# Optimization experiments

Measured on AMD Instinct MI355X. Metric: run time of the kernel, lower is better.

Reference implementation:

```python
import jax, jax.numpy as jnp
import numpy as np
from jax import lax

M = 8   # num_heads
K = 4   # num_points


def conv2d(x, w, b, pad):
    # x: [B,C,H,W], w: [O,I,kh,kw]
    y = lax.conv_general_dilated(x, w, (1, 1), [(pad, pad), (pad, pad)],
                                 dimension_numbers=('NCHW', 'OIHW', 'NCHW'))
    return y + b[None, :, None, None]


def grid_sample_zeros(v, px, py):
    # Bilinear grid_sample, align_corners=True, padding_mode='zeros'.
    # v: [N,Cm,H,W]; px,py: [N,P] in pixel coordinates.
    N, Cm, H, W = v.shape
    x0 = jnp.floor(px); y0 = jnp.floor(py)
    x1 = x0 + 1.0;      y1 = y0 + 1.0
    wx = px - x0;       wy = py - y0
    vflat = v.reshape(N, Cm, H * W)

    def tap(xi, yi):
        valid = (xi >= 0) & (xi <= W - 1) & (yi >= 0) & (yi <= H - 1)
        xc = jnp.clip(xi, 0, W - 1).astype(jnp.int32)
        yc = jnp.clip(yi, 0, H - 1).astype(jnp.int32)
        idx = yc * W + xc                          # [N,P]
        g = jnp.take_along_axis(vflat, idx[:, None, :], axis=2)  # [N,Cm,P]
        return g * valid[:, None, :].astype(v.dtype)

    v00 = tap(x0, y0); v01 = tap(x1, y0)
    v10 = tap(x0, y1); v11 = tap(x1, y1)
    wx = wx[:, None, :]; wy = wy[:, None, :]
    return (v00 * (1 - wx) * (1 - wy) + v01 * wx * (1 - wy)
            + v10 * (1 - wx) * wy + v11 * wx * wy)


def setup_inputs() -> dict:
    key = jax.random.key(0)
    ks = jax.random.split(key, 16)
    B, C, H, W = 8, 256, 64, 64
    s = 0.02
    inp = {
        'f_recalib': jax.random.normal(ks[0], (B, C, H, W), jnp.float32),
        'f_orig':    jax.random.normal(ks[1], (B, C, H, W), jnp.float32),
        'offset_w': jax.random.normal(ks[2], (M * K * 2, C, 3, 3), jnp.float32) * s,
        'offset_b': jnp.zeros((M * K * 2,), jnp.float32),
        'attn_w':   jax.random.normal(ks[3], (M * K, C, 3, 3), jnp.float32) * s,
        'attn_b':   jnp.zeros((M * K,), jnp.float32),
        'value_w':  jax.random.normal(ks[4], (C, C, 1, 1), jnp.float32) * s,
        'value_b':  jnp.zeros((C,), jnp.float32),
        'proj_w':   jax.random.normal(ks[5], (C, C, 1, 1), jnp.float32) * s,
        'proj_b':   jnp.zeros((C,), jnp.float32),
        'mlp_w1':   jax.random.normal(ks[6], (2 * C, C, 1, 1), jnp.float32) * s,
        'mlp_b1':   jnp.zeros((2 * C,), jnp.float32),
        'mlp_w2':   jax.random.normal(ks[7], (C, 2 * C, 1, 1), jnp.float32) * s,
        'mlp_b2':   jnp.zeros((C,), jnp.float32),
    }
    return inp


def reference(f_recalib, f_orig, offset_w, offset_b, attn_w, attn_b,
              value_w, value_b, proj_w, proj_b,
              mlp_w1, mlp_b1, mlp_w2, mlp_b2):
    B, C, H, W = f_recalib.shape
    Cm = C // M

    offsets = conv2d(f_recalib, offset_w, offset_b, 1).reshape(B, M, K, 2, H, W)
    attn = conv2d(f_recalib, attn_w, attn_b, 1).reshape(B, M, K, H, W)
    attn = jax.nn.softmax(attn, axis=2)
    value = conv2d(f_recalib, value_w, value_b, 0)

    gy, gx = jnp.meshgrid(jnp.arange(H, dtype=jnp.float32),
                          jnp.arange(W, dtype=jnp.float32), indexing='ij')
    gx_sym = (W - 1) - gx  # horizontally mirrored x coordinate
    # pixel-space sampling locations (align_corners=True normalization is exactly
    # inverted by grid_sample's unnormalization, so work in pixel coords)
    px = gx_sym[None, None, None] + offsets[:, :, :, 0]  # [B,M,K,H,W]
    py = gy[None, None, None] + offsets[:, :, :, 1]

    v = value.reshape(B * M, Cm, H, W)
    sampled = grid_sample_zeros(v, px.reshape(B * M, -1), py.reshape(B * M, -1))
    sampled = sampled.reshape(B, M, Cm, K, H, W)

    out = (sampled * attn[:, :, None]).sum(axis=3).reshape(B, C, H, W)
    out = conv2d(out, proj_w, proj_b, 0) + f_orig
    h = jax.nn.relu(conv2d(out, mlp_w1, mlp_b1, 0))
    out = conv2d(h, mlp_w2, mlp_b2, 0) + out
    return out
```

## Files before the change

### kernel.cpp

```cpp
#include <hip/hip_runtime.h>
#include <cstddef>

#define P_ 4096
#define PW_ 66

using u16 = unsigned short;
typedef float  f32x4  __attribute__((ext_vector_type(4)));
typedef u16    u16x8  __attribute__((ext_vector_type(8)));
typedef u16    u16x4  __attribute__((ext_vector_type(4)));
typedef __bf16 bf16x8 __attribute__((ext_vector_type(8)));

#define DEVINL __device__ __forceinline__

DEVINL u16 f2bf(float f) {
    union { float f; unsigned u; } v; v.f = f;
    unsigned r = v.u + 0x7fffu + ((v.u >> 16) & 1u);
    return (u16)(r >> 16);
}
DEVINL float bf2f(u16 h) {
    union { unsigned u; float f; } v; v.u = ((unsigned)h) << 16;
    return v.f;
}

DEVINL f32x4 mfma16(u16x8 a, u16x8 b, f32x4 c) {
    return __builtin_amdgcn_mfma_f32_16x16x32_bf16(
        __builtin_bit_cast(bf16x8, a), __builtin_bit_cast(bf16x8, b), c, 0, 0, 0);
}

DEVINL void gload16(const u16* src, const u16* lds_dst) {
    __builtin_amdgcn_global_load_lds(
        (const __attribute__((address_space(1))) void*)src,
        (__attribute__((address_space(3))) void*)lds_dst, 16, 0, 0);
}

__global__ void prep_weights(const float* __restrict__ off_w, const float* __restrict__ attn_w,
                             const float* __restrict__ val_w, const float* __restrict__ proj_w,
                             const float* __restrict__ w1, const float* __restrict__ w2,
                             u16* __restrict__ wbf) {
    int idx = blockIdx.x * 256 + threadIdx.x;
    if (idx >= 614400) return;
    float v;
    if (idx < 221184) {
        int tap = idx / 24576, rem = idx - tap * 24576, oc = rem >> 8, ic = rem & 255;
        v = (oc < 64) ? off_w[(size_t)(oc * 256 + ic) * 9 + tap]
                      : attn_w[(size_t)((oc - 64) * 256 + ic) * 9 + tap];
    } else if (idx < 286720) v = val_w[idx - 221184];
    else if (idx < 352256)   v = proj_w[idx - 286720];
    else if (idx < 483328)   v = w1[idx - 352256];
    else                     v = w2[idx - 483328];
    wbf[idx] = f2bf(v);
}

__global__ __launch_bounds__(256) void zero_pad(u16* __restrict__ xp) {
    const int b = blockIdx.x, t = threadIdx.x;
    const u16x8 z = (u16x8){0, 0, 0, 0, 0, 0, 0, 0};
    for (int q = t; q < 8320; q += 256) {
        const int p = q >> 5, chunk = q & 31;
        int row, col;
        if (p < 66)       { row = 0;  col = p; }
        else if (p < 132) { row = 65; col = p - 66; }
        else { const int q2 = p - 132; row = 1 + (q2 >> 1); col = (q2 & 1) * 65; }
        *(u16x8*)&xp[((size_t)(b * PW_ + row) * PW_ + col) * 256 + chunk * 8] = z;
    }
}

__global__ __launch_bounds__(256) void to_nhwc_pad(const float* __restrict__ in,
                                                   u16* __restrict__ xp) {
    const int y = blockIdx.x, c0 = blockIdx.y * 64, b = blockIdx.z;
    __shared__ u16 ts[64 * 72];
    const int t = threadIdx.x, cl = t >> 4, xq = t & 15;
    #pragma unroll
    for (int r = 0; r < 4; ++r) {
        const int c = r * 16 + cl;
        const float4 v = *(const float4*)&in[((size_t)(b * 256 + c0 + c)) * P_ + y * 64 + xq * 4];
        ts[(xq * 4 + 0) * 72 + c] = f2bf(v.x);
        ts[(xq * 4 + 1) * 72 + c] = f2bf(v.y);
        ts[(xq * 4 + 2) * 72 + c] = f2bf(v.z);
        ts[(xq * 4 + 3) * 72 + c] = f2bf(v.w);
    }
    __syncthreads();
    const int px = t >> 2, seg = t & 3;
    u16x8 o0, o1;
    #pragma unroll
    for (int j = 0; j < 8; ++j) {
        o0[j] = ts[px * 72 + seg * 16 + j];
        o1[j] = ts[px * 72 + seg * 16 + 8 + j];
    }
    const size_t base = ((size_t)(b * PW_ + y + 1) * PW_ + 1 + px) * 256 + c0 + seg * 16;
    *(u16x8*)&xp[base]     = o0;
    *(u16x8*)&xp[base + 8] = o1;
}

__global__ __launch_bounds__(256, 4) void conv3x3_mfma(
    const u16* __restrict__ xp, const u16* __restrict__ wconv,
    const float* __restrict__ off_b, const float* __restrict__ attn_b,
    u16* __restrict__ convout) {
    const int y = blockIdx.x, b = blockIdx.y;
    const int tid = threadIdx.x, w = tid >> 6, lane = tid & 63, g = lane >> 4, i = lane & 15;
    const int wm = w & 1, wn = w >> 1;
    const int srow = lane >> 4, sc = lane & 15;
    __shared__ u16 xs[64 * 128];
    __shared__ u16 wsL[96 * 128];

    f32x4 acc[2][3];
    #pragma unroll
    for (int mi = 0; mi < 2; ++mi)
        #pragma unroll
        for (int nj = 0; nj < 3; ++nj) acc[mi][nj] = (f32x4){0.f, 0.f, 0.f, 0.f};

    for (int tap = 0; tap < 9; ++tap) {
        const int dy = tap / 3, dx = tap % 3;
        const u16* xrow = xp + ((size_t)(b * PW_ + y + dy) * PW_ + dx) * 256;
        const u16* wt = wconv + (size_t)(tap * 96) * 256;
        for (int cc = 0; cc < 2; ++cc) {
            const int kc = cc * 128;
            #pragma unroll
            for (int t = 0; t < 4; ++t) {
                const int j = w * 4 + t;
                const int row = j * 4 + srow;
                const int cs = sc ^ (row & 7);
                gload16(xrow + (size_t)row * 256 + kc + (cs << 3), &xs[j * 512]);
            }
            #pragma unroll
            for (int t = 0; t < 6; ++t) {
                const int j = w * 6 + t;
                const int row = j * 4 + srow;
                const int cs = sc ^ (row & 7);
                gload16(wt + (size_t)row * 256 + kc + (cs << 3), &wsL[j * 512]);
            }
            __syncthreads();
            #pragma unroll
            for (int ks = 0; ks < 4; ++ks) {
                u16x8 a[2], bb[3];
                #pragma unroll
                for (int mi = 0; mi < 2; ++mi) {
                    const int pr = wm * 32 + mi * 16 + i;
                    a[mi] = *(const u16x8*)&xs[pr * 128 + (((ks * 4 + g) ^ (pr & 7)) << 3)];
                }
                #pragma unroll
                for (int nj = 0; nj < 3; ++nj) {
                    const int ocr = wn * 48 + nj * 16 + i;
                    bb[nj] = *(const u16x8*)&wsL[ocr * 128 + (((ks * 4 + g) ^ (ocr & 7)) << 3)];
                }
                #pragma unroll
                for (int mi = 0; mi < 2; ++mi)
                    #pragma unroll
                    for (int nj = 0; nj < 3; ++nj)
                        acc[mi][nj] = mfma16(a[mi], bb[nj], acc[mi][nj]);
            }
            __syncthreads();
        }
    }
    #pragma unroll
    for (int mi = 0; mi < 2; ++mi) {
        const int x0 = wm * 32 + mi * 16 + g * 4;
        #pragma unroll
        for (int nj = 0; nj < 3; ++nj) {
            const int oc = wn * 48 + nj * 16 + i;
            const float bv = (oc < 64) ? off_b[oc] : attn_b[oc - 64];
            #pragma unroll
            for (int r = 0; r < 4; ++r)
                convout[((size_t)(b * P_ + y * 64 + x0 + r)) * 96 + oc] =
                    f2bf(acc[mi][nj][r] + bv);
        }
    }
}

__global__ __launch_bounds__(256, 2) void gemm128(
    const u16* __restrict__ X, const u16* __restrict__ W,
    const float* __restrict__ bias, const float* __restrict__ resid,
    void* __restrict__ outp, u16* __restrict__ out_nhwc,
    const int KTOT, const int OC, const int mode, const int padded) {
    const int px0 = blockIdx.x * 128, oc0 = blockIdx.y * 128, b = blockIdx.z;
    const int tid = threadIdx.x, w = tid >> 6, lane = tid & 63, g = lane >> 4, i = lane & 15;
    const int wm = w & 1, wn = w >> 1;
    __shared__ u16 lds[32768];
    u16* xs = lds;
    u16* wsL = lds + 16384;

    f32x4 acc[4][4];
    #pragma unroll
    for (int mi = 0; mi < 4; ++mi)
        #pragma unroll
        for (int nj = 0; nj < 4; ++nj) acc[mi][nj] = (f32x4){0.f, 0.f, 0.f, 0.f};

    const int srow = (lane >> 4), sc = lane & 15;
    for (int kc = 0; kc < KTOT; kc += 128) {
        #pragma unroll
        for (int t = 0; t < 8; ++t) {
            const int j = w * 8 + t;
            const int row = j * 4 + srow;
            const int cs = sc ^ (row & 7);
            const u16* srcA;
            if (padded) {
                const int pxg = px0 + row;
                srcA = X + ((size_t)(b * PW_ + (pxg >> 6) + 1) * PW_ + (pxg & 63) + 1) * 256
                         + kc + (cs << 3);
            } else {
                srcA = X + (size_t)(b * P_ + px0 + row) * KTOT + kc + (cs << 3);
            }
            gload16(srcA, &xs[j * 512]);
        }
        #pragma unroll
        for (int t = 0; t < 8; ++t) {
            const int j = w * 8 + t;
            const int row = j * 4 + srow;
            const int cs = sc ^ (row & 7);
            gload16(W + (size_t)(oc0 + row) * KTOT + kc + (cs << 3), &wsL[j * 512]);
        }
        __syncthreads();
        #pragma unroll
        for (int ks = 0; ks < 4; ++ks) {
            u16x8 a[4], bb[4];
            #pragma unroll
            for (int mi = 0; mi < 4; ++mi) {
                const int px = wm * 64 + mi * 16 + i;
                a[mi] = *(const u16x8*)&xs[px * 128 + (((ks * 4 + g) ^ (px & 7)) << 3)];
            }
            #pragma unroll
            for (int nj = 0; nj < 4; ++nj) {
                const int oc = wn * 64 + nj * 16 + i;
                bb[nj] = *(const u16x8*)&wsL[oc * 128 + (((ks * 4 + g) ^ (oc & 7)) << 3)];
            }
            #pragma unroll
            for (int mi = 0; mi < 4; ++mi)
                #pragma unroll
                for (int nj = 0; nj < 4; ++nj)
                    acc[mi][nj] = mfma16(a[mi], bb[nj], acc[mi][nj]);
        }
        __syncthreads();
    }

    if (mode < 2) {
        u16* out = (u16*)outp;
        #pragma unroll
        for (int mi = 0; mi < 4; ++mi) {
            #pragma unroll
            for (int nj = 0; nj < 4; ++nj) {
                const int ocg = oc0 + wn * 64 + nj * 16 + i;
                const float bv = bias[ocg];
                #pragma unroll
                for (int r = 0; r < 4; ++r) {
                    const int px = px0 + wm * 64 + mi * 16 + g * 4 + r;
                    float v = acc[mi][nj][r] + bv;
                    if (mode == 1) v = fmaxf(v, 0.f);
                    out[((size_t)(b * P_ + px)) * OC + ocg] = f2bf(v);
                }
            }
        }
    } else {
        float* lf = (float*)lds;
        float* out = (float*)outp;
        #pragma unroll
        for (int h = 0; h < 2; ++h) {
            if (wm == h) {
                #pragma unroll
                for (int mi = 0; mi < 4; ++mi)
                    #pragma unroll
                    for (int nj = 0; nj < 4; ++nj) {
                        const int ocl = wn * 64 + nj * 16 + i;
                        const float bv = bias[oc0 + ocl];
                        #pragma unroll
                        for (int r = 0; r < 4; ++r)
                            lf[ocl * 66 + mi * 16 + g * 4 + r] = acc[mi][nj][r] + bv;
                    }
            }
            __syncthreads();
            {
                const int ocl = tid >> 1, sh = (tid & 1) * 32;
                const size_t base = ((size_t)b * OC + oc0 + ocl) * P_ + px0 + h * 64 + sh;
                #pragma unroll
                for (int q = 0; q < 8; ++q) {
                    const float4 r4 = *(const float4*)&resid[base + q * 4];
                    float4 o;
                    o.x = lf[ocl * 66 + sh + q * 4 + 0] + r4.x;
                    o.y = lf[ocl * 66 + sh + q * 4 + 1] + r4.y;
                    o.z = lf[ocl * 66 + sh + q * 4 + 2] + r4.z;
                    o.w = lf[ocl * 66 + sh + q * 4 + 3] + r4.w;
                    *(float4*)&out[base + q * 4] = o;
                    if (mode == 3) {
                        lf[ocl * 66 + sh + q * 4 + 0] = o.x;
                        lf[ocl * 66 + sh + q * 4 + 1] = o.y;
                        lf[ocl * 66 + sh + q * 4 + 2] = o.z;
                        lf[ocl * 66 + sh + q * 4 + 3] = o.w;
                    }
                }
            }
            if (mode == 3) {
                __syncthreads();
                const int pxl = tid >> 2, seg = tid & 3;
                const size_t b2 = ((size_t)(b * P_ + px0 + h * 64 + pxl)) * OC + oc0 + seg * 32;
                #pragma unroll
                for (int t = 0; t < 4; ++t) {
                    u16x8 o8;
                    #pragma unroll
                    for (int j = 0; j < 8; ++j)
                        o8[j] = f2bf(lf[(seg * 32 + t * 8 + j) * 66 + pxl]);
                    *(u16x8*)&out_nhwc[b2 + t * 8] = o8;
                }
            }
            __syncthreads();
        }
    }
}

__global__ __launch_bounds__(256) void sample_attend_bf(
    const u16* __restrict__ value, const u16* __restrict__ conv,
    u16* __restrict__ out1) {
    const int y = blockIdx.x, m = blockIdx.y, b = blockIdx.z;
    const int tid = threadIdx.x, x = tid >> 2, gq = tid & 3;
    const size_t prow = (size_t)(b * P_ + y * 64 + x);

    const u16x8 ov = *(const u16x8*)&conv[prow * 96 + m * 8];
    const u16x4 av = *(const u16x4*)&conv[prow * 96 + 64 + m * 4];

    float a[4];
    #pragma unroll
    for (int k = 0; k < 4; ++k) a[k] = bf2f(av[k]);
    const float mx = fmaxf(fmaxf(a[0], a[1]), fmaxf(a[2], a[3]));
    float s = 0.f;
    #pragma unroll
    for (int k = 0; k < 4; ++k) { a[k] = __expf(a[k] - mx); s += a[k]; }
    const float inv = 1.f / s;

    float acc[8];
    #pragma unroll
    for (int j = 0; j < 8; ++j) acc[j] = 0.f;

    const u16* vb = value + ((size_t)b * P_) * 256 + m * 32 + gq * 8;

    #pragma unroll
    for (int k = 0; k < 4; ++k) {
        const float offx = bf2f(ov[2 * k]), offy = bf2f(ov[2 * k + 1]);
        const float px = (float)(63 - x) + offx;
        const float py = (float)y + offy;
        const float x0f = floorf(px), y0f = floorf(py);
        const int xi0 = (int)x0f, yi0 = (int)y0f;
        const float wx = px - x0f, wy = py - y0f;
        const int xi1 = xi0 + 1, yi1 = yi0 + 1;
        const bool vx0 = (xi0 >= 0) & (xi0 <= 63), vx1 = (xi1 >= 0) & (xi1 <= 63);
        const bool vy0 = (yi0 >= 0) & (yi0 <= 63), vy1 = (yi1 >= 0) & (yi1 <= 63);
        const int cx0 = min(max(xi0, 0), 63), cx1 = min(max(xi1, 0), 63);
        const int cy0 = min(max(yi0, 0), 63), cy1 = min(max(yi1, 0), 63);
        const float ak = a[k] * inv;
        const float c00 = ak * (1.f - wx) * (1.f - wy) * ((vx0 & vy0) ? 1.f : 0.f);
        const float c01 = ak * wx * (1.f - wy) * ((vx1 & vy0) ? 1.f : 0.f);
        const float c10 = ak * (1.f - wx) * wy * ((vx0 & vy1) ? 1.f : 0.f);
        const float c11 = ak * wx * wy * ((vx1 & vy1) ? 1.f : 0.f);
        const u16x8 v00 = *(const u16x8*)&vb[(size_t)(cy0 * 64 + cx0) * 256];
        const u16x8 v01 = *(const u16x8*)&vb[(size_t)(cy0 * 64 + cx1) * 256];
        const u16x8 v10 = *(const u16x8*)&vb[(size_t)(cy1 * 64 + cx0) * 256];
        const u16x8 v11 = *(const u16x8*)&vb[(size_t)(cy1 * 64 + cx1) * 256];
        #pragma unroll
        for (int j = 0; j < 8; ++j)
            acc[j] += c00 * bf2f(v00[j]) + c01 * bf2f(v01[j])
                    + c10 * bf2f(v10[j]) + c11 * bf2f(v11[j]);
    }
    u16x8 o;
    #pragma unroll
    for (int j = 0; j < 8; ++j) o[j] = f2bf(acc[j]);
    *(u16x8*)&out1[prow * 256 + m * 32 + gq * 8] = o;
}

extern "C" void kernel_launch(void* const* d_in, const int* in_sizes, int n_in,
                              void* d_out, int out_size, void* d_ws, size_t ws_size,
                              hipStream_t stream) {
    const float* f_recalib = (const float*)d_in[0];
    const float* f_orig    = (const float*)d_in[1];
    const float* offset_w  = (const float*)d_in[2];
    const float* offset_b  = (const float*)d_in[3];
    const float* attn_w    = (const float*)d_in[4];
    const float* attn_b    = (const float*)d_in[5];
    const float* value_w   = (const float*)d_in[6];
    const float* value_b   = (const float*)d_in[7];
    const float* proj_w    = (const float*)d_in[8];
    const float* proj_b    = (const float*)d_in[9];
    const float* mlp_w1    = (const float*)d_in[10];
    const float* mlp_b1    = (const float*)d_in[11];
    const float* mlp_w2    = (const float*)d_in[12];
    const float* mlp_b2    = (const float*)d_in[13];
    float* out = (float*)d_out;

    u16* wsb      = (u16*)d_ws;
    u16* x_pad    = wsb;
    u16* convout  = wsb + 8921088;
    u16* value_bf = wsb + 12066816;
    u16* out1_bf  = wsb + 20455424;
    u16* wbf      = wsb + 28844032;
    u16* out2_bf  = x_pad;
    u16* h_bf     = wsb + 8921088;

    u16* wconv = wbf;
    u16* wval  = wbf + 221184;
    u16* wproj = wbf + 286720;
    u16* wmlp1 = wbf + 352256;
    u16* wmlp2 = wbf + 483328;

    prep_weights<<<2400, 256, 0, stream>>>(offset_w, attn_w, value_w, proj_w,
                                           mlp_w1, mlp_w2, wbf);
    zero_pad<<<8, 256, 0, stream>>>(x_pad);
    to_nhwc_pad<<<dim3(64, 4, 8), 256, 0, stream>>>(f_recalib, x_pad);
    conv3x3_mfma<<<dim3(64, 8), 256, 0, stream>>>(x_pad, wconv, offset_b, attn_b, convout);
    gemm128<<<dim3(32, 2, 8), 256, 0, stream>>>(x_pad, wval, value_b, nullptr,
                                                value_bf, nullptr, 256, 256, 0, 1);
    sample_attend_bf<<<dim3(64, 8, 8), 256, 0, stream>>>(value_bf, convout, out1_bf);
    gemm128<<<dim3(32, 2, 8), 256, 0, stream>>>(out1_bf, wproj, proj_b, f_orig,
                                                out, out2_bf, 256, 256, 3, 0);
    gemm128<<<dim3(32, 4, 8), 256, 0, stream>>>(out2_bf, wmlp1, mlp_b1, nullptr,
                                                h_bf, nullptr, 256, 512, 1, 0);
    gemm128<<<dim3(32, 2, 8), 256, 0, stream>>>(h_bf, wmlp2, mlp_b2, out,
                                                out, nullptr, 512, 256, 2, 0);
}
```

Before: 167.1 us.

## Double-buffer GEMM K-chunks and keep the intermediate residual in bf16

The 1x1-conv GEMM now splits K into 64-wide chunks, stages the next chunk into a second LDS buffer while the current one is computed, and uses explicit vmcnt waits and barriers. All output modes now write through an LDS transpose, so the bf16 NHWC stores are coalesced. The proj GEMM writes the intermediate residual as a bf16 NCHW copy instead of fp32 to the final output, and the last GEMM reads that bf16 residual. This cuts global traffic and overlaps loads with MFMA, at the cost of bf16 rounding on the residual path.

New measurement: 150.1 us. 1.11x faster.

```diff
diff --git a/kernel.cpp b/kernel.cpp
--- a/kernel.cpp
+++ b/kernel.cpp
@@ -166,10 +166,10 @@
     }
 }
 
-__global__ __launch_bounds__(256, 2) void gemm128(
+__global__ __launch_bounds__(256, 2) void gemm_dbuf(
     const u16* __restrict__ X, const u16* __restrict__ W,
-    const float* __restrict__ bias, const float* __restrict__ resid,
-    void* __restrict__ outp, u16* __restrict__ out_nhwc,
+    const float* __restrict__ bias, const void* __restrict__ resid,
+    void* __restrict__ outA, u16* __restrict__ outB,
     const int KTOT, const int OC, const int mode, const int padded) {
     const int px0 = blockIdx.x * 128, oc0 = blockIdx.y * 128, b = blockIdx.z;
     const int tid = threadIdx.x, w = tid >> 6, lane = tid & 63, g = lane >> 4, i = lane & 15;
@@ -178,49 +178,60 @@
     u16* xs = lds;
     u16* wsL = lds + 16384;
 
+    const int srcC = (lane & 7) ^ ((lane >> 3) & 7);
+
     f32x4 acc[4][4];
     #pragma unroll
     for (int mi = 0; mi < 4; ++mi)
         #pragma unroll
         for (int nj = 0; nj < 4; ++nj) acc[mi][nj] = (f32x4){0.f, 0.f, 0.f, 0.f};
 
-    const int srow = (lane >> 4), sc = lane & 15;
-    for (int kc = 0; kc < KTOT; kc += 128) {
-        #pragma unroll
-        for (int t = 0; t < 8; ++t) {
-            const int j = w * 8 + t;
-            const int row = j * 4 + srow;
-            const int cs = sc ^ (row & 7);
-            const u16* srcA;
+    const int NC = KTOT >> 6;
+
+    auto stage = [&](int buf, int kc) {
+        #pragma unroll
+        for (int t = 0; t < 4; ++t) {
+            const int j = w * 4 + t;
+            const int row = j * 8 + (lane >> 3);
+            const u16* sx;
             if (padded) {
                 const int pxg = px0 + row;
-                srcA = X + ((size_t)(b * PW_ + (pxg >> 6) + 1) * PW_ + (pxg & 63) + 1) * 256
-                         + kc + (cs << 3);
+                sx = X + ((size_t)(b * PW_ + (pxg >> 6) + 1) * PW_ + (pxg & 63) + 1) * 256
+                       + kc + (srcC << 3);
             } else {
-                srcA = X + (size_t)(b * P_ + px0 + row) * KTOT + kc + (cs << 3);
-            }
-            gload16(srcA, &xs[j * 512]);
-        }
-        #pragma unroll
-        for (int t = 0; t < 8; ++t) {
-            const int j = w * 8 + t;
-            const int row = j * 4 + srow;
-            const int cs = sc ^ (row & 7);
-            gload16(W + (size_t)(oc0 + row) * KTOT + kc + (cs << 3), &wsL[j * 512]);
-        }
-        __syncthreads();
-        #pragma unroll
-        for (int ks = 0; ks < 4; ++ks) {
+                sx = X + (size_t)(b * P_ + px0 + row) * KTOT + kc + (srcC << 3);
+            }
+            gload16(sx, &xs[buf * 8192 + j * 512]);
+        }
+        #pragma unroll
+        for (int t = 0; t < 4; ++t) {
+            const int j = w * 4 + t;
+            const int row = j * 8 + (lane >> 3);
+            gload16(W + (size_t)(oc0 + row) * KTOT + kc + (srcC << 3),
+                    &wsL[buf * 8192 + j * 512]);
+        }
+    };
+
+    stage(0, 0);
+    stage(1, 64);
+    asm volatile("s_waitcnt vmcnt(8)" ::: "memory");
+    __builtin_amdgcn_s_barrier();
+
+    for (int c = 0; c < NC; ++c) {
+        const u16* xb = &xs[(c & 1) * 8192];
+        const u16* wb = &wsL[(c & 1) * 8192];
+        #pragma unroll
+        for (int ks = 0; ks < 2; ++ks) {
             u16x8 a[4], bb[4];
             #pragma unroll
             for (int mi = 0; mi < 4; ++mi) {
-                const int px = wm * 64 + mi * 16 + i;
-                a[mi] = *(const u16x8*)&xs[px * 128 + (((ks * 4 + g) ^ (px & 7)) << 3)];
+                const int row = wm * 64 + mi * 16 + i;
+                a[mi] = *(const u16x8*)&xb[row * 64 + (((ks * 4 + g) ^ (row & 7)) << 3)];
             }
             #pragma unroll
             for (int nj = 0; nj < 4; ++nj) {
-                const int oc = wn * 64 + nj * 16 + i;
-                bb[nj] = *(const u16x8*)&wsL[oc * 128 + (((ks * 4 + g) ^ (oc & 7)) << 3)];
+                const int row = wn * 64 + nj * 16 + i;
+                bb[nj] = *(const u16x8*)&wb[row * 64 + (((ks * 4 + g) ^ (row & 7)) << 3)];
             }
             #pragma unroll
             for (int mi = 0; mi < 4; ++mi)
@@ -228,79 +239,94 @@
                 for (int nj = 0; nj < 4; ++nj)
                     acc[mi][nj] = mfma16(a[mi], bb[nj], acc[mi][nj]);
         }
-        __syncthreads();
-    }
-
-    if (mode < 2) {
-        u16* out = (u16*)outp;
-        #pragma unroll
-        for (int mi = 0; mi < 4; ++mi) {
+        __builtin_amdgcn_sched_barrier(0);
+        __builtin_amdgcn_s_barrier();
+        if (c + 2 < NC) {
+            stage(c & 1, (c + 2) << 6);
+            asm volatile("s_waitcnt vmcnt(8)" ::: "memory");
+        } else {
+            asm volatile("s_waitcnt vmcnt(0)" ::: "memory");
+        }
+        __builtin_amdgcn_s_barrier();
+    }
+
+    float* lf = (float*)lds;
+    const int pxq = tid >> 2, segq = tid & 3;
+    const int oclh = tid >> 1, shh = (tid & 1) * 32;
+
+    #pragma unroll
+    for (int h = 0; h < 2; ++h) {
+        if (wm == h) {
             #pragma unroll
             for (int nj = 0; nj < 4; ++nj) {
-                const int ocg = oc0 + wn * 64 + nj * 16 + i;
-                const float bv = bias[ocg];
-                #pragma unroll
-                for (int r = 0; r < 4; ++r) {
-                    const int px = px0 + wm * 64 + mi * 16 + g * 4 + r;
-                    float v = acc[mi][nj][r] + bv;
-                    if (mode == 1) v = fmaxf(v, 0.f);
-                    out[((size_t)(b * P_ + px)) * OC + ocg] = f2bf(v);
-                }
-            }
-        }
-    } else {
-        float* lf = (float*)lds;
-        float* out = (float*)outp;
-        #pragma unroll
-        for (int h = 0; h < 2; ++h) {
-            if (wm == h) {
+                const int ocl = wn * 64 + nj * 16 + i;
+                const float bv = bias[oc0 + ocl];
                 #pragma unroll
                 for (int mi = 0; mi < 4; ++mi)
                     #pragma unroll
-                    for (int nj = 0; nj < 4; ++nj) {
-                        const int ocl = wn * 64 + nj * 16 + i;
-                        const float bv = bias[oc0 + ocl];
-                        #pragma unroll
-                        for (int r = 0; r < 4; ++r)
-                            lf[ocl * 66 + mi * 16 + g * 4 + r] = acc[mi][nj][r] + bv;
-                    }
+                    for (int r = 0; r < 4; ++r)
+                        lf[ocl * 66 + mi * 16 + g * 4 + r] = acc[mi][nj][r] + bv;
+            }
+        }
+        __syncthreads();
+        const int pxg0 = px0 + h * 64;
+
+        if (mode == 4) {
+            const float* rf = (const float*)resid;
+            const size_t rb = ((size_t)b * 256 + oc0 + oclh) * P_ + pxg0 + shh;
+            #pragma unroll
+            for (int q = 0; q < 8; ++q) {
+                const float4 r4 = *(const float4*)&rf[rb + q * 4];
+                lf[oclh * 66 + shh + q * 4 + 0] += r4.x;
+                lf[oclh * 66 + shh + q * 4 + 1] += r4.y;
+                lf[oclh * 66 + shh + q * 4 + 2] += r4.z;
+                lf[oclh * 66 + shh + q * 4 + 3] += r4.w;
             }
             __syncthreads();
-            {
-                const int ocl = tid >> 1, sh = (tid & 1) * 32;
-                const size_t base = ((size_t)b * OC + oc0 + ocl) * P_ + px0 + h * 64 + sh;
-                #pragma unroll
-                for (int q = 0; q < 8; ++q) {
-                    const float4 r4 = *(const float4*)&resid[base + q * 4];
-                    float4 o;
-                    o.x = lf[ocl * 66 + sh + q * 4 + 0] + r4.x;
-                    o.y = lf[ocl * 66 + sh + q * 4 + 1] + r4.y;
-                    o.z = lf[ocl * 66 + sh + q * 4 + 2] + r4.z;
-                    o.w = lf[ocl * 66 + sh + q * 4 + 3] + r4.w;
-                    *(float4*)&out[base + q * 4] = o;
-                    if (mode == 3) {
-                        lf[ocl * 66 + sh + q * 4 + 0] = o.x;
-                        lf[ocl * 66 + sh + q * 4 + 1] = o.y;
-                        lf[ocl * 66 + sh + q * 4 + 2] = o.z;
-                        lf[ocl * 66 + sh + q * 4 + 3] = o.w;
-                    }
+        }
+
+        if (mode <= 1 || mode == 4) {
+            const size_t nb = ((size_t)(b * P_ + pxg0 + pxq)) * OC + oc0 + segq * 32;
+            #pragma unroll
+            for (int t2 = 0; t2 < 4; ++t2) {
+                u16x8 o8;
+                #pragma unroll
+                for (int jj = 0; jj < 8; ++jj) {
+                    float v = lf[(segq * 32 + t2 * 8 + jj) * 66 + pxq];
+                    if (mode == 1) v = fmaxf(v, 0.f);
+                    o8[jj] = f2bf(v);
                 }
-            }
-            if (mode == 3) {
-                __syncthreads();
-                const int pxl = tid >> 2, seg = tid & 3;
-                const size_t b2 = ((size_t)(b * P_ + px0 + h * 64 + pxl)) * OC + oc0 + seg * 32;
-                #pragma unroll
-                for (int t = 0; t < 4; ++t) {
-                    u16x8 o8;
-                    #pragma unroll
-                    for (int j = 0; j < 8; ++j)
-                        o8[j] = f2bf(lf[(seg * 32 + t * 8 + j) * 66 + pxl]);
-                    *(u16x8*)&out_nhwc[b2 + t * 8] = o8;
-                }
-            }
-            __syncthreads();
-        }
+                *(u16x8*)&outB[nb + t2 * 8] = o8;
+            }
+        }
+        if (mode == 4) {
+            u16* on = (u16*)outA;
+            const size_t cb = ((size_t)b * 256 + oc0 + oclh) * P_ + pxg0 + shh;
+            #pragma unroll
+            for (int t2 = 0; t2 < 4; ++t2) {
+                u16x8 o8;
+                #pragma unroll
+                for (int jj = 0; jj < 8; ++jj)
+                    o8[jj] = f2bf(lf[oclh * 66 + shh + t2 * 8 + jj]);
+                *(u16x8*)&on[cb + t2 * 8] = o8;
+            }
+        }
+        if (mode == 5) {
+            const u16* rb16 = (const u16*)resid;
+            float* of = (float*)outA;
+            const size_t cb = ((size_t)b * 256 + oc0 + oclh) * P_ + pxg0 + shh;
+            #pragma unroll
+            for (int q = 0; q < 8; ++q) {
+                const u16x4 r4 = *(const u16x4*)&rb16[cb + q * 4];
+                float4 o;
+                o.x = lf[oclh * 66 + shh + q * 4 + 0] + bf2f(r4[0]);
+                o.y = lf[oclh * 66 + shh + q * 4 + 1] + bf2f(r4[1]);
+                o.z = lf[oclh * 66 + shh + q * 4 + 2] + bf2f(r4[2]);
+                o.w = lf[oclh * 66 + shh + q * 4 + 3] + bf2f(r4[3]);
+                *(float4*)&of[cb + q * 4] = o;
+            }
+        }
+        __syncthreads();
     }
 }
 
@@ -381,14 +407,15 @@
     const float* mlp_b2    = (const float*)d_in[13];
     float* out = (float*)d_out;
 
-    u16* wsb      = (u16*)d_ws;
-    u16* x_pad    = wsb;
-    u16* convout  = wsb + 8921088;
-    u16* value_bf = wsb + 12066816;
-    u16* out1_bf  = wsb + 20455424;
-    u16* wbf      = wsb + 28844032;
-    u16* out2_bf  = x_pad;
-    u16* h_bf     = wsb + 8921088;
+    u16* wsb       = (u16*)d_ws;
+    u16* x_pad     = wsb;
+    u16* convout   = wsb + 8921088;
+    u16* value_bf  = wsb + 12066816;
+    u16* out1_bf   = wsb + 20455424;
+    u16* wbf       = wsb + 28844032;
+    u16* out2_nchw = wsb + 29458432;
+    u16* out2_bf   = x_pad;
+    u16* h_bf      = wsb + 8921088;
 
     u16* wconv = wbf;
     u16* wval  = wbf + 221184;
@@ -401,13 +428,13 @@
     zero_pad<<<8, 256, 0, stream>>>(x_pad);
     to_nhwc_pad<<<dim3(64, 4, 8), 256, 0, stream>>>(f_recalib, x_pad);
     conv3x3_mfma<<<dim3(64, 8), 256, 0, stream>>>(x_pad, wconv, offset_b, attn_b, convout);
-    gemm128<<<dim3(32, 2, 8), 256, 0, stream>>>(x_pad, wval, value_b, nullptr,
-                                                value_bf, nullptr, 256, 256, 0, 1);
+    gemm_dbuf<<<dim3(32, 2, 8), 256, 0, stream>>>(x_pad, wval, value_b, nullptr,
+                                                  nullptr, value_bf, 256, 256, 0, 1);
     sample_attend_bf<<<dim3(64, 8, 8), 256, 0, stream>>>(value_bf, convout, out1_bf);
-    gemm128<<<dim3(32, 2, 8), 256, 0, stream>>>(out1_bf, wproj, proj_b, f_orig,
-                                                out, out2_bf, 256, 256, 3, 0);
-    gemm128<<<dim3(32, 4, 8), 256, 0, stream>>>(out2_bf, wmlp1, mlp_b1, nullptr,
-                                                h_bf, nullptr, 256, 512, 1, 0);
-    gemm128<<<dim3(32, 2, 8), 256, 0, stream>>>(h_bf, wmlp2, mlp_b2, out,
-                                                out, nullptr, 512, 256, 2, 0);
-}
+    gemm_dbuf<<<dim3(32, 2, 8), 256, 0, stream>>>(out1_bf, wproj, proj_b, f_orig,
+                                                  out2_nchw, out2_bf, 256, 256, 4, 0);
+    gemm_dbuf<<<dim3(32, 4, 8), 256, 0, stream>>>(out2_bf, wmlp1, mlp_b1, nullptr,
+                                                  nullptr, h_bf, 256, 512, 1, 0);
+    gemm_dbuf<<<dim3(32, 2, 8), 256, 0, stream>>>(h_bf, wmlp2, mlp_b2, out2_nchw,
+                                                  out, nullptr, 512, 256, 5, 0);
+}
```
